# Performance work log

Hardware: AMD Instinct MI355X
Metric: run time of the kernel (lower is better)

## Reference

```python
import jax, jax.numpy as jnp
import numpy as np

N = 4096      # total instances in the bag
S = 64        # number of images (segments), idx_list has S+1 boundaries
L = 500
D = 128
FLAT = 50 * 4 * 4  # 800


def _conv(x, w, b):
    # x: [N,C,H,W], w: [O,I,5,5], VALID conv, stride 1
    y = jax.lax.conv_general_dilated(x, w, (1, 1), 'VALID',
                                     dimension_numbers=('NCHW', 'OIHW', 'NCHW'))
    return y + b[None, :, None, None]


def _maxpool2(x):
    return jax.lax.reduce_window(x, -jnp.inf, jax.lax.max,
                                 (1, 1, 2, 2), (1, 1, 2, 2), 'VALID')


def setup_inputs() -> dict:
    key = jax.random.key(0)
    ks = jax.random.split(key, 18)
    def p(k, shape, fan):
        return jax.random.normal(k, shape, jnp.float32) * np.float32(1.0 / np.sqrt(fan))
    x = jax.random.normal(ks[0], (1, N, 3, 28, 28), jnp.float32)
    idx_list = (jnp.arange(S + 1, dtype=jnp.int32) * (N // S))  # sorted boundaries 0..N
    return {
        'x': x,
        'idx_list': idx_list,
        'conv1_w': p(ks[1], (20, 3, 5, 5), 3 * 25), 'conv1_b': jnp.zeros((20,), jnp.float32),
        'conv2_w': p(ks[2], (50, 20, 5, 5), 20 * 25), 'conv2_b': jnp.zeros((50,), jnp.float32),
        'fc_w': p(ks[3], (FLAT, L), FLAT), 'fc_b': jnp.zeros((L,), jnp.float32),
        'a1_w1': p(ks[4], (L, D), L), 'a1_b1': jnp.zeros((D,), jnp.float32),
        'a1_w2': p(ks[5], (D, 1), D), 'a1_b2': jnp.zeros((1,), jnp.float32),
        'a2_w1': p(ks[6], (L, D), L), 'a2_b1': jnp.zeros((D,), jnp.float32),
        'a2_w2': p(ks[7], (D, 1), D), 'a2_b2': jnp.zeros((1,), jnp.float32),
        'clf_w': p(ks[8], (L, 1), L), 'clf_b': jnp.zeros((1,), jnp.float32),
    }


def reference(x, idx_list, conv1_w, conv1_b, conv2_w, conv2_b, fc_w, fc_b,
              a1_w1, a1_b1, a1_w2, a1_b2, a2_w1, a2_b1, a2_w2, a2_b2,
              clf_w, clf_b):
    xs = x[0]                                         # squeeze(0): [N,3,28,28]
    h = _maxpool2(jax.nn.relu(_conv(xs, conv1_w, conv1_b)))   # [N,20,12,12]
    h = _maxpool2(jax.nn.relu(_conv(h, conv2_w, conv2_b)))    # [N,50,4,4]
    H = jax.nn.relu(h.reshape(-1, FLAT) @ fc_w + fc_b)        # [N,L]

    def attn1(z):
        return jnp.tanh(z @ a1_w1 + a1_b1) @ a1_w2 + a1_b2    # [.,1]

    A = attn1(H).T                                    # [1,N] (returned raw, pre-softmax)

    # ragged per-segment softmax pooling (replaces the Python loop)
    n = H.shape[0]
    seg = jnp.searchsorted(idx_list[1:], jnp.arange(n, dtype=idx_list.dtype), side='right')
    a = attn1(H)[:, 0]                                # [N] scores (same math as per-segment recompute)
    seg_max = jax.ops.segment_max(a, seg, num_segments=S)
    e = jnp.exp(a - seg_max[seg])
    denom = jax.ops.segment_sum(e, seg, num_segments=S)
    w = e / denom[seg]                                # per-segment softmax weights
    instance_f = jax.ops.segment_sum(w[:, None] * H, seg, num_segments=S)  # [S,L]

    b_att = jnp.tanh(instance_f @ a2_w1 + a2_b1) @ a2_w2 + a2_b2  # [S,1]
    B = jax.nn.softmax(b_att[:, 0])[None, :]          # [1,S]
    bag_feature = B @ instance_f                      # [1,L]
    Y_prob = jax.nn.sigmoid(bag_feature @ clf_w + clf_b)  # [1,1]
    Y_hat = (Y_prob >= 0.5).astype(jnp.float32)
    return (Y_prob, Y_hat, A)
```

## Files before the change

### kernel.cpp

```cpp
#include <hip/hip_runtime.h>
#include <math.h>

typedef _Float16 f16x8 __attribute__((ext_vector_type(8)));
typedef float    f32x4 __attribute__((ext_vector_type(4)));

static __device__ __forceinline__ unsigned short f2h(float f) {
  _Float16 h = (_Float16)f;
  return __builtin_bit_cast(unsigned short, h);
}
static __device__ __forceinline__ unsigned int pk_max(unsigned int a, unsigned int b) {
  unsigned int d;
  asm("v_pk_max_f16 %0, %1, %2" : "=v"(d) : "v"(a), "v"(b));
  return d;
}
static __device__ __forceinline__ unsigned int pk_add(unsigned int a, unsigned int b) {
  unsigned int d;
  asm("v_pk_add_f16 %0, %1, %2" : "=v"(d) : "v"(a), "v"(b));
  return d;
}
static __device__ __forceinline__ unsigned int pkh2(float lo, float hi) {
  return (unsigned int)f2h(lo) | ((unsigned int)f2h(hi) << 16);
}

__global__ __launch_bounds__(256) void k_prep_all(const float* __restrict__ c1w,
                                                  const float* __restrict__ c2w,
                                                  const float* __restrict__ fcw,
                                                  const float* __restrict__ a1w1,
                                                  unsigned short* __restrict__ Wc1g,
                                                  unsigned short* __restrict__ Wg,
                                                  unsigned short* __restrict__ Wtfc,
                                                  unsigned short* __restrict__ Wt1) {
  int i = blockIdx.x * 256 + threadIdx.x;
  if (i < 6400) {
    int kh = i / 1280, r = i % 1280;
    int co = r / 40, q = r % 40;
    int kw = q >> 2, ci = q & 3;
    Wc1g[i] = f2h((co < 20 && ci < 3 && kw < 5) ? c1w[((co * 3 + ci) * 5 + kh) * 5 + kw] : 0.f);
    return;
  }
  i -= 6400;
  if (i < 38400) {
    int tap = i / 1536, r = i % 1536;
    int co = r / 24, ci = r % 24;
    Wg[i] = f2h((co < 50 && ci < 20) ? c2w[(co * 20 + ci) * 25 + tap] : 0.f);
    return;
  }
  i -= 38400;
  if (i < 409600) {
    int kt = i >> 14, r = i & 16383;
    int nn = r >> 5, kk = r & 31;
    int k = kt * 32 + kk;
    Wtfc[i] = f2h((nn < 500) ? fcw[k * 500 + nn] : 0.f);
    return;
  }
  i -= 409600;
  if (i < 65536) {
    int kt = i >> 12, r = i & 4095;
    int col = r >> 5, kk = r & 31;
    int k = kt * 32 + kk;
    Wt1[i] = f2h((k < 500) ? a1w1[k * 128 + col] : 0.f);
  }
}

__global__ __launch_bounds__(128, 2) void k_conv12(const float* __restrict__ x,
                                                   const unsigned short* __restrict__ Wc1g,
                                                   const float* __restrict__ cb1,
                                                   const unsigned short* __restrict__ Wg,
                                                   const float* __restrict__ cb2,
                                                   unsigned short* __restrict__ flat16) {
  __shared__ unsigned short xcl[3200];
  __shared__ unsigned short h1s[3472];
  int tid = threadIdx.x;
  int n = blockIdx.x;
  int w = tid >> 6;
  int lane = tid & 63;
  int r16 = lane & 15, g = lane >> 4;

  if (tid < 16) h1s[3456 + tid] = 0;
  if (tid < 64) xcl[3136 + tid] = 0;
  {
    const float* xg = x + (size_t)n * 2352;
    float v0[7], v1[7], v2[7];
    #pragma unroll
    for (int i = 0; i < 7; ++i) {
      int p = tid + i * 128;
      if (p < 784) { v0[i] = xg[p]; v1[i] = xg[784 + p]; v2[i] = xg[1568 + p]; }
    }
    #pragma unroll
    for (int i = 0; i < 7; ++i) {
      int p = tid + i * 128;
      if (p < 784) {
        uint2 vv; vv.x = pkh2(v0[i], v1[i]); vv.y = (unsigned int)f2h(v2[i]);
        *(uint2*)(xcl + 4 * p) = vv;
      }
    }
  }
  __syncthreads();

  {
    f16x8 bv[5][2];
    #pragma unroll
    for (int kh = 0; kh < 5; kh++) {
      bv[kh][0] = __builtin_bit_cast(f16x8, *(const uint4*)(Wc1g + (kh * 32 + r16) * 40 + 8 * g));
      bv[kh][1] = __builtin_bit_cast(f16x8, *(const uint4*)(Wc1g + (kh * 32 + 16 + r16) * 40 + 8 * g));
    }
    float bias0 = cb1[r16];
    float bias1 = (r16 < 4) ? cb1[16 + r16] : 0.f;
    unsigned int b2_0 = pkh2(bias0, bias0);
    unsigned int b2_1 = pkh2(bias1, bias1);
    int ay = (r16 >> 3), ax = (r16 & 7) + 2 * g;
    const unsigned short* xlane = xcl + (ay * 28 + ax) * 4;

    auto do_chunk = [&](const int chunk) {
      f32x4 acc[4][2];
      #pragma unroll
      for (int ti = 0; ti < 4; ti++) {
        acc[ti][0] = (f32x4){0.f, 0.f, 0.f, 0.f};
        acc[ti][1] = (f32x4){0.f, 0.f, 0.f, 0.f};
      }
      #pragma unroll
      for (int kh = 0; kh < 5; kh++) {
        #pragma unroll
        for (int ti = 0; ti < 4; ti++) {
          const int t = chunk * 4 + ti;
          const int ty = t / 3, tx = t - ty * 3;
          const unsigned short* p = xlane + ((2 * ty + kh) * 28 + 8 * tx) * 4;
          uint2 lo = *(const uint2*)p;
          uint2 hi = *(const uint2*)(p + 4);
          uint4 af; af.x = lo.x; af.y = lo.y; af.z = hi.x; af.w = hi.y;
          f16x8 av = __builtin_bit_cast(f16x8, af);
          acc[ti][0] = __builtin_amdgcn_mfma_f32_16x16x32_f16(av, bv[kh][0], acc[ti][0], 0, 0, 0);
          acc[ti][1] = __builtin_amdgcn_mfma_f32_16x16x32_f16(av, bv[kh][1], acc[ti][1], 0, 0, 0);
        }
      }
      #pragma unroll
      for (int ti = 0; ti < 4; ti++) {
        const int t = chunk * 4 + ti;
        const int ty = t / 3, tx = t - ty * 3;
        #pragma unroll
        for (int nt = 0; nt < 2; nt++) {
          int co = 16 * nt + r16;
          f32x4 c = acc[ti][nt];
          unsigned int pk = pkh2(fmaxf(c[0], c[1]), fmaxf(c[2], c[3]));
          unsigned int other = (unsigned int)__shfl_xor((int)pk, 32);
          unsigned int m2 = pk_max(pk, other);
          unsigned int r2 = pk_max(pk_add(m2, nt ? b2_1 : b2_0), 0u);
          if (g < 2 && co < 24) {
            int px0 = 4 * tx + 2 * g;
            unsigned short* o = h1s + (ty * 12 + px0) * 24 + co;
            o[0]  = (unsigned short)r2;
            o[24] = (unsigned short)(r2 >> 16);
          }
        }
      }
    };
    if (w == 0) { do_chunk(0); do_chunk(2); do_chunk(4); do_chunk(6); do_chunk(8); }
    else        { do_chunk(1); do_chunk(3); do_chunk(5); do_chunk(7); }
  }
  __syncthreads();

  {
    unsigned int cbp[4];
    cbp[0] = pkh2(cb2[r16], cb2[r16]);
    cbp[1] = pkh2(cb2[16 + r16], cb2[16 + r16]);
    cbp[2] = pkh2(cb2[32 + r16], cb2[32 + r16]);
    float cb3 = (r16 < 2) ? cb2[48 + r16] : 0.f;
    cbp[3] = pkh2(cb3, cb3);

    const unsigned short* Ab[2];
    #pragma unroll
    for (int mtp = 0; mtp < 2; mtp++) {
      int posl = (2 * w + mtp) * 16 + r16;
      int oy = posl >> 3, ox = posl & 7;
      Ab[mtp] = h1s + (oy * 12 + ox) * 24 + 8 * g;
    }
    const unsigned short* Bb = Wg + r16 * 24 + 8 * g;

    f32x4 acc[2][4];
    #pragma unroll
    for (int mt = 0; mt < 2; mt++)
      #pragma unroll
      for (int nt = 0; nt < 4; nt++) acc[mt][nt] = (f32x4){0.f, 0.f, 0.f, 0.f};

    uint4 FAa[2], FAb[4], FBa[2], FBb[4];
    auto lf = [&](uint4* A, uint4* B, const int tap) {
      const int kh = tap / 5, kw = tap % 5;
      const int dA = (kh * 12 + kw) * 24;
      const int dB = tap * 1536;
      #pragma unroll
      for (int nt = 0; nt < 4; nt++) {
        uint4 u = make_uint4(0, 0, 0, 0);
        if (g < 3) u = *(const uint4*)(Bb + dB + nt * 384);
        B[nt] = u;
      }
      A[0] = *(const uint4*)(Ab[0] + dA);
      A[1] = *(const uint4*)(Ab[1] + dA);
    };
    auto mma = [&](const uint4* A, const uint4* B) {
      #pragma unroll
      for (int mt = 0; mt < 2; mt++) {
        f16x8 av = __builtin_bit_cast(f16x8, A[mt]);
        #pragma unroll
        for (int nt = 0; nt < 4; nt++) {
          acc[mt][nt] = __builtin_amdgcn_mfma_f32_16x16x32_f16(
              av, __builtin_bit_cast(f16x8, B[nt]), acc[mt][nt], 0, 0, 0);
        }
      }
    };

    lf(FAa, FAb, 0);
    #pragma unroll
    for (int tap = 0; tap < 25; tap += 2) {
      if (tap + 1 < 25) lf(FBa, FBb, tap + 1);
      mma(FAa, FAb);
      if (tap + 2 < 25) lf(FAa, FAb, tap + 2);
      if (tap + 1 < 25) mma(FBa, FBb);
    }

    #pragma unroll
    for (int mtp = 0; mtp < 2; mtp++) {
      int py = 2 * w + mtp;
      #pragma unroll
      for (int nt = 0; nt < 4; nt++) {
        int co = 16 * nt + r16;
        f32x4 c = acc[mtp][nt];
        unsigned int pk = pkh2(fmaxf(c[0], c[1]), fmaxf(c[2], c[3]));
        unsigned int other = (unsigned int)__shfl_xor((int)pk, 32);
        unsigned int m2 = pk_max(pk, other);
        unsigned int r2 = pk_max(pk_add(m2, cbp[nt]), 0u);
        if (g < 2 && co < 50) {
          *(unsigned int*)(flat16 + ((size_t)n * 50 + co) * 16 + py * 4 + 2 * g) = r2;
        }
      }
    }
  }
}

__global__ __launch_bounds__(256) void k_fc_mfma(const unsigned short* __restrict__ flat16,
                                                 const unsigned short* __restrict__ Wt,
                                                 const float* __restrict__ b,
                                                 float* __restrict__ H,
                                                 unsigned short* __restrict__ H16) {
  int tid = threadIdx.x;
  int wave = tid >> 6, lane = tid & 63;
  int r16 = lane & 15, g = lane >> 4;
  int bm = blockIdx.x & 15, bn = blockIdx.x >> 4;
  int m0 = bm * 256 + wave * 64;
  int n0 = bn * 32;

  f32x4 acc[4][2];
  #pragma unroll
  for (int mt = 0; mt < 4; mt++) {
    acc[mt][0] = (f32x4){0.f, 0.f, 0.f, 0.f};
    acc[mt][1] = (f32x4){0.f, 0.f, 0.f, 0.f};
  }

  const unsigned short* Abase = flat16 + (size_t)(m0 + r16) * 800 + 8 * g;
  const unsigned short* Bbase = Wt + (size_t)(n0 + r16) * 32 + 8 * g;

  for (int kt = 0; kt < 25; kt++) {
    uint4 bf0 = *(const uint4*)(Bbase + kt * 16384);
    uint4 bf1 = *(const uint4*)(Bbase + kt * 16384 + 512);
    f16x8 bv0 = __builtin_bit_cast(f16x8, bf0);
    f16x8 bv1 = __builtin_bit_cast(f16x8, bf1);
    #pragma unroll
    for (int mt = 0; mt < 4; mt++) {
      uint4 af = *(const uint4*)(Abase + mt * 12800 + kt * 32);
      f16x8 av = __builtin_bit_cast(f16x8, af);
      acc[mt][0] = __builtin_amdgcn_mfma_f32_16x16x32_f16(av, bv0, acc[mt][0], 0, 0, 0);
      acc[mt][1] = __builtin_amdgcn_mfma_f32_16x16x32_f16(av, bv1, acc[mt][1], 0, 0, 0);
    }
  }

  #pragma unroll
  for (int nt = 0; nt < 2; nt++) {
    int col = n0 + nt * 16 + r16;
    bool real = col < 500;
    float bias = real ? b[col] : 0.f;
    #pragma unroll
    for (int mt = 0; mt < 4; mt++) {
      #pragma unroll
      for (int j = 0; j < 4; j++) {
        int row = m0 + mt * 16 + 4 * g + j;
        float val = fmaxf(acc[mt][nt][j] + bias, 0.f);
        if (real) H[(size_t)row * 500 + col] = val;
        H16[(size_t)row * 512 + col] = f2h(val);
      }
    }
  }
}

__global__ __launch_bounds__(64) void k_attn1_mfma(const unsigned short* __restrict__ H16,
                                                   const unsigned short* __restrict__ Wt1,
                                                   const float* __restrict__ b1,
                                                   const float* __restrict__ w2,
                                                   const float* __restrict__ b2,
                                                   float* __restrict__ a,
                                                   float* __restrict__ outA) {
  int lane = threadIdx.x;
  int r16 = lane & 15, g = lane >> 4;
  int m0 = blockIdx.x * 32;

  f32x4 acc[2][8];
  #pragma unroll
  for (int mt = 0; mt < 2; mt++)
    #pragma unroll
    for (int nt = 0; nt < 8; nt++) acc[mt][nt] = (f32x4){0.f, 0.f, 0.f, 0.f};

  const unsigned short* Abase = H16 + (size_t)(m0 + r16) * 512 + 8 * g;
  const unsigned short* Bbase = Wt1 + r16 * 32 + 8 * g;

  for (int kt = 0; kt < 16; kt++) {
    uint4 a0 = *(const uint4*)(Abase + kt * 32);
    uint4 a1 = *(const uint4*)(Abase + 16 * 512 + kt * 32);
    f16x8 av0 = __builtin_bit_cast(f16x8, a0);
    f16x8 av1 = __builtin_bit_cast(f16x8, a1);
    #pragma unroll
    for (int nt = 0; nt < 8; nt++) {
      uint4 bf = *(const uint4*)(Bbase + kt * 4096 + nt * 512);
      f16x8 bv = __builtin_bit_cast(f16x8, bf);
      acc[0][nt] = __builtin_amdgcn_mfma_f32_16x16x32_f16(av0, bv, acc[0][nt], 0, 0, 0);
      acc[1][nt] = __builtin_amdgcn_mfma_f32_16x16x32_f16(av1, bv, acc[1][nt], 0, 0, 0);
    }
  }

  float b1v[8], w2v[8];
  #pragma unroll
  for (int nt = 0; nt < 8; nt++) {
    int col = nt * 16 + r16;
    b1v[nt] = b1[col];
    w2v[nt] = w2[col];
  }
  float bb2 = b2[0];

  #pragma unroll
  for (int mt = 0; mt < 2; mt++) {
    float part[4];
    #pragma unroll
    for (int j = 0; j < 4; j++) {
      float s = 0.f;
      #pragma unroll
      for (int nt = 0; nt < 8; nt++)
        s += tanhf(acc[mt][nt][j] + b1v[nt]) * w2v[nt];
      part[j] = s;
    }
    #pragma unroll
    for (int off = 1; off < 16; off <<= 1) {
      #pragma unroll
      for (int j = 0; j < 4; j++) part[j] += __shfl_xor(part[j], off);
    }
    if (r16 == 0) {
      #pragma unroll
      for (int j = 0; j < 4; j++) {
        int row = m0 + mt * 16 + 4 * g + j;
        float val = part[j] + bb2;
        a[row] = val;
        outA[row] = val;
      }
    }
  }
}

__global__ __launch_bounds__(512) void k_segbatt(const float* __restrict__ a,
                                                 const float* __restrict__ H,
                                                 const int* __restrict__ idx,
                                                 const float* __restrict__ w1,
                                                 const float* __restrict__ b1,
                                                 const float* __restrict__ w2,
                                                 const float* __restrict__ b2,
                                                 float* __restrict__ instf,
                                                 float* __restrict__ batt) {
  __shared__ float fs[500];
  __shared__ float part[512];
  __shared__ float pool[4][500];
  __shared__ float red[8];
  __shared__ float sval;
  int s = blockIdx.x, tid = threadIdx.x;
  int i0 = idx[s], i1 = idx[s + 1];

  float mx = -INFINITY;
  for (int i = i0 + tid; i < i1; i += 512) mx = fmaxf(mx, a[i]);
  #pragma unroll
  for (int off = 32; off > 0; off >>= 1) mx = fmaxf(mx, __shfl_down(mx, off));
  if ((tid & 63) == 0) red[tid >> 6] = mx;
  __syncthreads();
  if (tid == 0) {
    float m2 = red[0];
    #pragma unroll
    for (int j = 1; j < 8; j++) m2 = fmaxf(m2, red[j]);
    sval = m2;
  }
  __syncthreads();
  float m = sval;
  float sm = 0.f;
  for (int i = i0 + tid; i < i1; i += 512) sm += expf(a[i] - m);
  #pragma unroll
  for (int off = 32; off > 0; off >>= 1) sm += __shfl_down(sm, off);
  if ((tid & 63) == 0) red[tid >> 6] = sm;
  __syncthreads();
  if (tid == 0) {
    float t2 = 0.f;
    #pragma unroll
    for (int j = 0; j < 8; j++) t2 += red[j];
    sval = t2;
  }
  __syncthreads();
  float inv = 1.f / sval;
  {
    int q = tid >> 7;
    int t = tid & 127;
    int len = i1 - i0;
    int lo = i0 + (len * q) / 4;
    int hi = i0 + (len * (q + 1)) / 4;
    if (t < 125) {
      float a0 = 0.f, a1 = 0.f, a2 = 0.f, a3 = 0.f;
      for (int i = lo; i < hi; i++) {
        float e = expf(a[i] - m) * inv;
        const float* Hr = H + (size_t)i * 500 + t;
        a0 += e * Hr[0];
        a1 += e * Hr[125];
        a2 += e * Hr[250];
        a3 += e * Hr[375];
      }
      pool[q][t]       = a0;
      pool[q][t + 125] = a1;
      pool[q][t + 250] = a2;
      pool[q][t + 375] = a3;
    }
  }
  __syncthreads();
  if (tid < 500) {
    float v = pool[0][tid] + pool[1][tid] + pool[2][tid] + pool[3][tid];
    instf[s * 500 + tid] = v;
    fs[tid] = v;
  }
  __syncthreads();
  int c = tid & 127, q = tid >> 7;
  float t = 0.f;
  int k0 = q * 125;
  #pragma unroll 5
  for (int k = k0; k < k0 + 125; k++) t += fs[k] * w1[k * 128 + c];
  part[tid] = t;
  __syncthreads();
  if (tid < 128) {
    float tt = part[tid] + part[tid + 128] + part[tid + 256] + part[tid + 384] + b1[tid];
    float v = tanhf(tt) * w2[tid];
    #pragma unroll
    for (int off = 32; off > 0; off >>= 1) v += __shfl_down(v, off);
    if ((tid & 63) == 0) red[tid >> 6] = v;
  }
  __syncthreads();
  if (tid == 0) batt[s] = red[0] + red[1] + b2[0];
}

__global__ __launch_bounds__(256) void k_final(const float* __restrict__ batt,
                                               const float* __restrict__ instf,
                                               const float* __restrict__ clfw,
                                               const float* __restrict__ clfb,
                                               float* __restrict__ out) {
  __shared__ float Bsh[64];
  __shared__ float red[4];
  int tid = threadIdx.x;
  if (tid < 64) {
    float v = batt[tid];
    float mx = v;
    #pragma unroll
    for (int off = 32; off > 0; off >>= 1) mx = fmaxf(mx, __shfl_xor(mx, off));
    float e = expf(v - mx);
    float smv = e;
    #pragma unroll
    for (int off = 32; off > 0; off >>= 1) smv += __shfl_xor(smv, off);
    Bsh[tid] = e / smv;
  }
  __syncthreads();
  float part = 0.f;
  if (tid < 250) {
    float bag0 = 0.f, bag1 = 0.f;
    #pragma unroll 4
    for (int s2 = 0; s2 < 64; s2++) {
      float Bv = Bsh[s2];
      bag0 += Bv * instf[s2 * 500 + tid];
      bag1 += Bv * instf[s2 * 500 + tid + 250];
    }
    part = bag0 * clfw[tid] + bag1 * clfw[tid + 250];
  }
  #pragma unroll
  for (int off = 32; off > 0; off >>= 1) part += __shfl_down(part, off);
  if ((tid & 63) == 0) red[tid >> 6] = part;
  __syncthreads();
  if (tid == 0) {
    float z = red[0] + red[1] + red[2] + red[3] + clfb[0];
    out[0] = 1.f / (1.f + expf(-z));
    out[1] = (z >= 0.f) ? 1.f : 0.f;
  }
}

extern "C" void kernel_launch(void* const* d_in, const int* in_sizes, int n_in,
                              void* d_out, int out_size, void* d_ws, size_t ws_size,
                              hipStream_t stream) {
  const float* x       = (const float*)d_in[0];
  const int*   idx     = (const int*)d_in[1];
  const float* conv1_w = (const float*)d_in[2];
  const float* conv1_b = (const float*)d_in[3];
  const float* conv2_w = (const float*)d_in[4];
  const float* conv2_b = (const float*)d_in[5];
  const float* fc_w    = (const float*)d_in[6];
  const float* fc_b    = (const float*)d_in[7];
  const float* a1_w1   = (const float*)d_in[8];
  const float* a1_b1   = (const float*)d_in[9];
  const float* a1_w2   = (const float*)d_in[10];
  const float* a1_b2   = (const float*)d_in[11];
  const float* a2_w1   = (const float*)d_in[12];
  const float* a2_b1   = (const float*)d_in[13];
  const float* a2_w2   = (const float*)d_in[14];
  const float* a2_b2   = (const float*)d_in[15];
  const float* clf_w   = (const float*)d_in[16];
  const float* clf_b   = (const float*)d_in[17];
  float* out = (float*)d_out;

  int N = in_sizes[0] / 2352;
  int S = in_sizes[1] - 1;

  float* wsf   = (float*)d_ws;
  float* H     = wsf;
  float* a     = H + (size_t)N * 500;
  float* instf = a + N;
  float* batt  = instf + (size_t)S * 500;
  unsigned short* Wg    = (unsigned short*)(batt + S + 8);
  unsigned short* Wc1g  = Wg + 38400;
  unsigned short* Wtfc  = Wc1g + 6400;
  unsigned short* Wt1   = Wtfc + 409600;
  unsigned short* flat16= Wt1 + 65536;
  unsigned short* H16   = flat16 + (size_t)N * 800;

  k_prep_all<<<2031, 256, 0, stream>>>(conv1_w, conv2_w, fc_w, a1_w1, Wc1g, Wg, Wtfc, Wt1);
  k_conv12<<<N, 128, 0, stream>>>(x, Wc1g, conv1_b, Wg, conv2_b, flat16);
  k_fc_mfma<<<256, 256, 0, stream>>>(flat16, Wtfc, fc_b, H, H16);
  k_attn1_mfma<<<N / 32, 64, 0, stream>>>(H16, Wt1, a1_b1, a1_w2, a1_b2, a, out + 2);
  k_segbatt<<<S, 512, 0, stream>>>(a, H, idx, a2_w1, a2_b1, a2_w2, a2_b2, instf, batt);
  k_final<<<1, 256, 0, stream>>>(batt, instf, clf_w, clf_b, out);
}
```

Measured before the change: 125.5 us.

## Widen conv block to four waves, swap fc grid order, halve attn tile

The fused conv kernel now runs 256 threads (4 waves) per image instead of 128. Conv1 chunks are spread over four waves, and conv2 work is split by output-channel tile instead of by row pair, so each wave does 4 M-tiles times 1 N-tile. This raises per-image parallelism and cuts per-wave register use, at the cost of redundant A-fragment LDS loads across waves. The fc kernel's block index now varies N fastest, for different L2 reuse, and the attention kernel uses 16-row tiles with twice as many blocks to improve occupancy.

```diff
diff --git a/kernel.cpp b/kernel.cpp
--- a/kernel.cpp
+++ b/kernel.cpp
@@ -62,7 +62,7 @@
   }
 }
 
-__global__ __launch_bounds__(128, 2) void k_conv12(const float* __restrict__ x,
+__global__ __launch_bounds__(256, 2) void k_conv12(const float* __restrict__ x,
                                                    const unsigned short* __restrict__ Wc1g,
                                                    const float* __restrict__ cb1,
                                                    const unsigned short* __restrict__ Wg,
@@ -80,15 +80,15 @@
   if (tid < 64) xcl[3136 + tid] = 0;
   {
     const float* xg = x + (size_t)n * 2352;
-    float v0[7], v1[7], v2[7];
-    #pragma unroll
-    for (int i = 0; i < 7; ++i) {
-      int p = tid + i * 128;
+    float v0[4], v1[4], v2[4];
+    #pragma unroll
+    for (int i = 0; i < 4; ++i) {
+      int p = tid + i * 256;
       if (p < 784) { v0[i] = xg[p]; v1[i] = xg[784 + p]; v2[i] = xg[1568 + p]; }
     }
     #pragma unroll
-    for (int i = 0; i < 7; ++i) {
-      int p = tid + i * 128;
+    for (int i = 0; i < 4; ++i) {
+      int p = tid + i * 256;
       if (p < 784) {
         uint2 vv; vv.x = pkh2(v0[i], v1[i]); vv.y = (unsigned int)f2h(v2[i]);
         *(uint2*)(xcl + 4 * p) = vv;
@@ -154,57 +154,49 @@
         }
       }
     };
-    if (w == 0) { do_chunk(0); do_chunk(2); do_chunk(4); do_chunk(6); do_chunk(8); }
-    else        { do_chunk(1); do_chunk(3); do_chunk(5); do_chunk(7); }
+    if      (w == 0) { do_chunk(0); do_chunk(4); do_chunk(8); }
+    else if (w == 1) { do_chunk(1); do_chunk(5); }
+    else if (w == 2) { do_chunk(2); do_chunk(6); }
+    else             { do_chunk(3); do_chunk(7); }
   }
   __syncthreads();
 
   {
-    unsigned int cbp[4];
-    cbp[0] = pkh2(cb2[r16], cb2[r16]);
-    cbp[1] = pkh2(cb2[16 + r16], cb2[16 + r16]);
-    cbp[2] = pkh2(cb2[32 + r16], cb2[32 + r16]);
-    float cb3 = (r16 < 2) ? cb2[48 + r16] : 0.f;
-    cbp[3] = pkh2(cb3, cb3);
-
-    const unsigned short* Ab[2];
-    #pragma unroll
-    for (int mtp = 0; mtp < 2; mtp++) {
-      int posl = (2 * w + mtp) * 16 + r16;
+    int co = 16 * w + r16;
+    float cbv = (co < 50) ? cb2[co] : 0.f;
+    unsigned int cbp = pkh2(cbv, cbv);
+
+    const unsigned short* Ab[4];
+    #pragma unroll
+    for (int mt = 0; mt < 4; mt++) {
+      int posl = mt * 16 + r16;
       int oy = posl >> 3, ox = posl & 7;
-      Ab[mtp] = h1s + (oy * 12 + ox) * 24 + 8 * g;
-    }
-    const unsigned short* Bb = Wg + r16 * 24 + 8 * g;
-
-    f32x4 acc[2][4];
-    #pragma unroll
-    for (int mt = 0; mt < 2; mt++)
-      #pragma unroll
-      for (int nt = 0; nt < 4; nt++) acc[mt][nt] = (f32x4){0.f, 0.f, 0.f, 0.f};
-
-    uint4 FAa[2], FAb[4], FBa[2], FBb[4];
-    auto lf = [&](uint4* A, uint4* B, const int tap) {
+      Ab[mt] = h1s + (oy * 12 + ox) * 24 + 8 * g;
+    }
+    const unsigned short* Bb = Wg + co * 24 + 8 * g;
+
+    f32x4 acc[4];
+    #pragma unroll
+    for (int mt = 0; mt < 4; mt++) acc[mt] = (f32x4){0.f, 0.f, 0.f, 0.f};
+
+    uint4 FAa[4], FBa[4];
+    uint4 FAb, FBb;
+    auto lf = [&](uint4* A, uint4& B, const int tap) {
       const int kh = tap / 5, kw = tap % 5;
       const int dA = (kh * 12 + kw) * 24;
       const int dB = tap * 1536;
+      uint4 u = make_uint4(0, 0, 0, 0);
+      if (g < 3) u = *(const uint4*)(Bb + dB);
+      B = u;
       #pragma unroll
-      for (int nt = 0; nt < 4; nt++) {
-        uint4 u = make_uint4(0, 0, 0, 0);
-        if (g < 3) u = *(const uint4*)(Bb + dB + nt * 384);
-        B[nt] = u;
-      }
-      A[0] = *(const uint4*)(Ab[0] + dA);
-      A[1] = *(const uint4*)(Ab[1] + dA);
+      for (int mt = 0; mt < 4; mt++) A[mt] = *(const uint4*)(Ab[mt] + dA);
     };
-    auto mma = [&](const uint4* A, const uint4* B) {
+    auto mma = [&](const uint4* A, const uint4& B) {
+      f16x8 bvv = __builtin_bit_cast(f16x8, B);
       #pragma unroll
-      for (int mt = 0; mt < 2; mt++) {
-        f16x8 av = __builtin_bit_cast(f16x8, A[mt]);
-        #pragma unroll
-        for (int nt = 0; nt < 4; nt++) {
-          acc[mt][nt] = __builtin_amdgcn_mfma_f32_16x16x32_f16(
-              av, __builtin_bit_cast(f16x8, B[nt]), acc[mt][nt], 0, 0, 0);
-        }
+      for (int mt = 0; mt < 4; mt++) {
+        acc[mt] = __builtin_amdgcn_mfma_f32_16x16x32_f16(
+            __builtin_bit_cast(f16x8, A[mt]), bvv, acc[mt], 0, 0, 0);
       }
     };
 
@@ -218,19 +210,14 @@
     }
 
     #pragma unroll
-    for (int mtp = 0; mtp < 2; mtp++) {
-      int py = 2 * w + mtp;
-      #pragma unroll
-      for (int nt = 0; nt < 4; nt++) {
-        int co = 16 * nt + r16;
-        f32x4 c = acc[mtp][nt];
-        unsigned int pk = pkh2(fmaxf(c[0], c[1]), fmaxf(c[2], c[3]));
-        unsigned int other = (unsigned int)__shfl_xor((int)pk, 32);
-        unsigned int m2 = pk_max(pk, other);
-        unsigned int r2 = pk_max(pk_add(m2, cbp[nt]), 0u);
-        if (g < 2 && co < 50) {
-          *(unsigned int*)(flat16 + ((size_t)n * 50 + co) * 16 + py * 4 + 2 * g) = r2;
-        }
+    for (int mt = 0; mt < 4; mt++) {
+      f32x4 c = acc[mt];
+      unsigned int pk = pkh2(fmaxf(c[0], c[1]), fmaxf(c[2], c[3]));
+      unsigned int other = (unsigned int)__shfl_xor((int)pk, 32);
+      unsigned int m2 = pk_max(pk, other);
+      unsigned int r2 = pk_max(pk_add(m2, cbp), 0u);
+      if (g < 2 && co < 50) {
+        *(unsigned int*)(flat16 + ((size_t)n * 50 + co) * 16 + mt * 4 + 2 * g) = r2;
       }
     }
   }
@@ -244,7 +231,7 @@
   int tid = threadIdx.x;
   int wave = tid >> 6, lane = tid & 63;
   int r16 = lane & 15, g = lane >> 4;
-  int bm = blockIdx.x & 15, bn = blockIdx.x >> 4;
+  int bn = blockIdx.x & 15, bm = blockIdx.x >> 4;
   int m0 = bm * 256 + wave * 64;
   int n0 = bn * 32;
 
@@ -299,28 +286,23 @@
                                                    float* __restrict__ outA) {
   int lane = threadIdx.x;
   int r16 = lane & 15, g = lane >> 4;
-  int m0 = blockIdx.x * 32;
-
-  f32x4 acc[2][8];
-  #pragma unroll
-  for (int mt = 0; mt < 2; mt++)
-    #pragma unroll
-    for (int nt = 0; nt < 8; nt++) acc[mt][nt] = (f32x4){0.f, 0.f, 0.f, 0.f};
+  int m0 = blockIdx.x * 16;
+
+  f32x4 acc[8];
+  #pragma unroll
+  for (int nt = 0; nt < 8; nt++) acc[nt] = (f32x4){0.f, 0.f, 0.f, 0.f};
 
   const unsigned short* Abase = H16 + (size_t)(m0 + r16) * 512 + 8 * g;
   const unsigned short* Bbase = Wt1 + r16 * 32 + 8 * g;
 
   for (int kt = 0; kt < 16; kt++) {
     uint4 a0 = *(const uint4*)(Abase + kt * 32);
-    uint4 a1 = *(const uint4*)(Abase + 16 * 512 + kt * 32);
     f16x8 av0 = __builtin_bit_cast(f16x8, a0);
-    f16x8 av1 = __builtin_bit_cast(f16x8, a1);
     #pragma unroll
     for (int nt = 0; nt < 8; nt++) {
       uint4 bf = *(const uint4*)(Bbase + kt * 4096 + nt * 512);
       f16x8 bv = __builtin_bit_cast(f16x8, bf);
-      acc[0][nt] = __builtin_amdgcn_mfma_f32_16x16x32_f16(av0, bv, acc[0][nt], 0, 0, 0);
-      acc[1][nt] = __builtin_amdgcn_mfma_f32_16x16x32_f16(av1, bv, acc[1][nt], 0, 0, 0);
+      acc[nt] = __builtin_amdgcn_mfma_f32_16x16x32_f16(av0, bv, acc[nt], 0, 0, 0);
     }
   }
 
@@ -333,30 +315,27 @@
   }
   float bb2 = b2[0];
 
-  #pragma unroll
-  for (int mt = 0; mt < 2; mt++) {
-    float part[4];
+  float part[4];
+  #pragma unroll
+  for (int j = 0; j < 4; j++) {
+    float s = 0.f;
+    #pragma unroll
+    for (int nt = 0; nt < 8; nt++)
+      s += tanhf(acc[nt][j] + b1v[nt]) * w2v[nt];
+    part[j] = s;
+  }
+  #pragma unroll
+  for (int off = 1; off < 16; off <<= 1) {
+    #pragma unroll
+    for (int j = 0; j < 4; j++) part[j] += __shfl_xor(part[j], off);
+  }
+  if (r16 == 0) {
     #pragma unroll
     for (int j = 0; j < 4; j++) {
-      float s = 0.f;
-      #pragma unroll
-      for (int nt = 0; nt < 8; nt++)
-        s += tanhf(acc[mt][nt][j] + b1v[nt]) * w2v[nt];
-      part[j] = s;
-    }
-    #pragma unroll
-    for (int off = 1; off < 16; off <<= 1) {
-      #pragma unroll
-      for (int j = 0; j < 4; j++) part[j] += __shfl_xor(part[j], off);
-    }
-    if (r16 == 0) {
-      #pragma unroll
-      for (int j = 0; j < 4; j++) {
-        int row = m0 + mt * 16 + 4 * g + j;
-        float val = part[j] + bb2;
-        a[row] = val;
-        outA[row] = val;
-      }
+      int row = m0 + 4 * g + j;
+      float val = part[j] + bb2;
+      a[row] = val;
+      outA[row] = val;
     }
   }
 }
@@ -534,9 +513,9 @@
   unsigned short* H16   = flat16 + (size_t)N * 800;
 
   k_prep_all<<<2031, 256, 0, stream>>>(conv1_w, conv2_w, fc_w, a1_w1, Wc1g, Wg, Wtfc, Wt1);
-  k_conv12<<<N, 128, 0, stream>>>(x, Wc1g, conv1_b, Wg, conv2_b, flat16);
+  k_conv12<<<N, 256, 0, stream>>>(x, Wc1g, conv1_b, Wg, conv2_b, flat16);
   k_fc_mfma<<<256, 256, 0, stream>>>(flat16, Wtfc, fc_b, H, H16);
-  k_attn1_mfma<<<N / 32, 64, 0, stream>>>(H16, Wt1, a1_b1, a1_w2, a1_b2, a, out + 2);
+  k_attn1_mfma<<<N / 16, 64, 0, stream>>>(H16, Wt1, a1_b1, a1_w2, a1_b2, a, out + 2);
   k_segbatt<<<S, 512, 0, stream>>>(a, H, idx, a2_w1, a2_b1, a2_w2, a2_b2, instf, batt);
   k_final<<<1, 256, 0, stream>>>(batt, instf, clf_w, clf_b, out);
 }
```

Result: slower. 148.7 us (+18.5%).
